# Kernel tuning notes

Measured on AMD Instinct MI355X. Metric: run time of the kernel, lower is better.

## Reference

```python
import jax, jax.numpy as jnp
import numpy as np

N, E = 50000, 800000
IN, H, C = 256, 8, 32  # heads=8, hidden_dim=32 -> out dim 256
NEG_SLOPE = 0.2
EPS = 1e-5


def setup_inputs() -> dict:
    key = jax.random.key(0)
    ks = jax.random.split(key, 6)
    x = jax.random.normal(ks[0], (N, IN), jnp.float32)
    edge_index = jax.random.randint(ks[1], (2, E), 0, N, dtype=jnp.int32)
    W = jax.random.normal(ks[2], (IN, H * C), jnp.float32) / np.sqrt(IN).astype(np.float32)
    att_src = jax.random.normal(ks[3], (H, C), jnp.float32) * 0.1
    att_dst = jax.random.normal(ks[4], (H, C), jnp.float32) * 0.1
    bias = jnp.zeros((H * C,), jnp.float32)
    gamma = jnp.ones((H * C,), jnp.float32)
    beta = jnp.zeros((H * C,), jnp.float32)
    return {"x": x, "edge_index": edge_index, "W": W, "att_src": att_src,
            "att_dst": att_dst, "bias": bias, "gamma": gamma, "beta": beta}


def reference(x, edge_index, W, att_src, att_dst, bias, gamma, beta):
    n = x.shape[0]
    # Linear projection -> per-head features [N, H, C]
    xl = (x @ W).reshape(n, H, C)
    # Per-node attention half-logits [N, H]
    a_src = jnp.einsum('nhc,hc->nh', xl, att_src)
    a_dst = jnp.einsum('nhc,hc->nh', xl, att_dst)
    # Add self loops (PyG GATConv default)
    loops = jnp.arange(n, dtype=edge_index.dtype)
    src = jnp.concatenate([edge_index[0], loops])  # [E+N]
    dst = jnp.concatenate([edge_index[1], loops])
    # Edge attention logits + segment softmax over destination neighborhoods
    logits = jax.nn.leaky_relu(a_src[src] + a_dst[dst], NEG_SLOPE)  # [E+N, H]
    seg_max = jax.ops.segment_max(logits, dst, num_segments=n)
    ex = jnp.exp(logits - seg_max[dst])
    denom = jax.ops.segment_sum(ex, dst, num_segments=n)
    alpha = ex / denom[dst]  # [E+N, H]
    # Weighted scatter-aggregation of source features
    msgs = xl[src] * alpha[:, :, None]  # [E+N, H, C]
    out = jax.ops.segment_sum(msgs, dst, num_segments=n).reshape(n, H * C) + bias
    # LayerNorm over feature dim
    mu = jnp.mean(out, axis=-1, keepdims=True)
    var = jnp.var(out, axis=-1, keepdims=True)
    return (out - mu) / jnp.sqrt(var + EPS) * gamma + beta
```

## Files before the change

kernel.cpp:

```cpp
#include <hip/hip_runtime.h>
#include <math.h>

#define NEG 0.2f
#define LNEPS 1e-5f
#define GB 512

typedef __attribute__((ext_vector_type(8))) short bf16x8;
typedef __attribute__((ext_vector_type(8))) unsigned short u16x8;
typedef __attribute__((ext_vector_type(4))) float f32x4;
typedef __attribute__((ext_vector_type(4))) unsigned int u32x4;

__device__ __forceinline__ float lrelu(float x){ return x > 0.f ? x : NEG*x; }

__device__ __forceinline__ short f2b(float f){
  unsigned u = __float_as_uint(f);
  unsigned r = u + 0x7fffu + ((u >> 16) & 1u);
  return (short)(r >> 16);
}
__device__ __forceinline__ float b2f(unsigned short u){
  return __uint_as_float(((unsigned)u) << 16);
}
__device__ __forceinline__ unsigned cvtpk(float lo, float hi){
  unsigned r;
  asm("v_cvt_pk_bf16_f32 %0, %1, %2" : "=v"(r) : "v"(lo), "v"(hi));
  return r;
}

__global__ __launch_bounds__(256) void wt_k(const float* __restrict__ W,
                                            const float* __restrict__ att_src,
                                            const float* __restrict__ att_dst,
                                            const int* __restrict__ dst,
                                            unsigned short* __restrict__ WTp,
                                            unsigned short* __restrict__ WSp,
                                            int* __restrict__ deg, int E){
  int b = blockIdx.x;
  int tid = threadIdx.x;
  if (b < 32){
    int g = b*256 + tid;
    int l = g & 63;
    int s = (g>>6) & 7;
    int j = (g>>9) & 3;
    int w = g >> 11;
    int col = w*64 + j*16 + (l & 15);
    int kb  = s*32 + (l>>4)*8;
    u16x8 v;
    #pragma unroll
    for (int e=0;e<8;e++) v[e] = (unsigned short)f2b(W[(size_t)(kb+e)*256 + col]);
    *(u16x8*)(WTp + (size_t)g*8) = v;
  } else if (b < 34){
    int g = (b-32)*256 + tid;
    int l = g & 63;
    int s = g >> 6;
    int col = l & 15;
    int kb  = s*32 + (l>>4)*8;
    int head = col & 7;
    const float* av = (col < 8 ? att_src : att_dst) + head*32;
    u16x8 v;
    #pragma unroll
    for (int e=0;e<8;e++){
      const float* wr = W + (size_t)(kb+e)*256 + head*32;
      float sum = 0.f;
      #pragma unroll
      for (int c2=0;c2<32;c2++) sum += wr[c2]*av[c2];
      v[e] = (unsigned short)f2b(sum);
    }
    *(u16x8*)(WSp + (size_t)g*8) = v;
  } else {
    int e = (b-34)*256 + tid;
    if (e < E) atomicAdd(&deg[dst[e]], 1);
  }
}

__global__ __launch_bounds__(1024) void scan1_k(const int* __restrict__ deg,
                                                int* __restrict__ off,
                                                int* __restrict__ bsum, int n){
  __shared__ int wsum[16];
  int tid=threadIdx.x, lane=tid&63, wid=tid>>6;
  int i = blockIdx.x*1024 + tid;
  int v = (i<n)?(deg[i]+1):0;
  int x = v;
  #pragma unroll
  for (int s=1;s<64;s<<=1){ int t2=__shfl_up(x,s); if (lane>=s) x+=t2; }
  if (lane==63) wsum[wid]=x;
  __syncthreads();
  if (tid<16){
    int y=wsum[tid];
    #pragma unroll
    for (int s=1;s<16;s<<=1){ int t2=__shfl_up(y,s); if (tid>=s) y+=t2; }
    wsum[tid]=y;
  }
  __syncthreads();
  int prefix=(wid? wsum[wid-1]:0);
  if (i<n) off[i]=prefix + x - v;
  if (tid==0) bsum[blockIdx.x]=wsum[15];
}

__global__ __launch_bounds__(1024) void scan3self_k(int* __restrict__ off,
    const int* __restrict__ bsum, int* __restrict__ sorted, int* __restrict__ cur,
    int n, int total){
  __shared__ int prefs;
  if (threadIdx.x < 64){
    int v = ((int)threadIdx.x < blockIdx.x) ? bsum[threadIdx.x] : 0;
    #pragma unroll
    for (int s=1;s<64;s<<=1) v += __shfl_xor(v, s);
    if (threadIdx.x==0) prefs = v;
  }
  __syncthreads();
  int i = blockIdx.x*1024 + threadIdx.x;
  if (blockIdx.x==0 && threadIdx.x==0) off[n] = total;
  if (i>=n) return;
  int o = off[i] + prefs;
  off[i] = o;
  sorted[o] = i;
  cur[i] = 1;
}

__device__ __forceinline__ void load_tile(float4 v[4], const float* __restrict__ A,
                                          int t, int M, int tid){
  const float* base = A + (size_t)t*4096;
  int rmax = M - 1 - t*16;
  #pragma unroll
  for (int j=0;j<4;j++){
    int idx4 = (j>>1)*512 + 2*tid + (j&1);
    int r = idx4 >> 6;
    if (r > rmax) idx4 = (rmax<<6) | (idx4 & 63);
    v[j] = *(const float4*)(base + (size_t)idx4*4);
  }
}

__global__ __launch_bounds__(256, 2) void gemm_scat_k(const float* __restrict__ A,
    const unsigned short* __restrict__ WTp, const unsigned short* __restrict__ WSp,
    unsigned short* __restrict__ Cb, float* __restrict__ asd, int M, int nTiles,
    const int* __restrict__ src, const int* __restrict__ dst,
    const int* __restrict__ off, int* __restrict__ cur,
    int* __restrict__ sorted, int E){
  __shared__ __align__(16) unsigned short Asb[16*256];
  int tid = threadIdx.x;

  if (blockIdx.x >= GB){
    int e = (blockIdx.x - GB)*256 + tid;
    if (e < E){
      int d = dst[e];
      int pos = off[d] + atomicAdd(&cur[d], 1);
      sorted[pos] = src[e];
    }
    return;
  }

  int w   = tid >> 6;
  int l   = tid & 63;
  int l15 = l & 15;
  int kg  = l >> 4;
  int colbase = w*64;

  bf16x8 bfr[4][8];
  #pragma unroll
  for (int j=0;j<4;j++)
    #pragma unroll
    for (int ks=0;ks<8;ks++)
      bfr[j][ks] = *(const bf16x8*)(WTp + ((size_t)(((w*4+j)*8+ks)*64 + l))*8);

  bf16x8 bfa[8];
  if (w==0){
    #pragma unroll
    for (int ks=0;ks<8;ks++)
      bfa[ks] = *(const bf16x8*)(WSp + ((size_t)(ks*64 + l))*8);
  }

  int t = blockIdx.x;
  if (t >= nTiles) return;
  float4 v[4];
  load_tile(v, A, t, M, tid);

  while (t < nTiles){
    __syncthreads();
    #pragma unroll
    for (int p=0;p<2;p++){
      u32x4 q;
      q.x = cvtpk(v[2*p].x,   v[2*p].y);
      q.y = cvtpk(v[2*p].z,   v[2*p].w);
      q.z = cvtpk(v[2*p+1].x, v[2*p+1].y);
      q.w = cvtpk(v[2*p+1].z, v[2*p+1].w);
      int slot = p*256 + tid;
      int sw = slot ^ ((slot>>5)&7);
      *(u32x4*)(Asb + (size_t)sw*8) = q;
    }
    __syncthreads();

    int tn = t + GB;
    if (tn < nTiles) load_tile(v, A, tn, M, tid);

    f32x4 acc[4];
    #pragma unroll
    for (int j=0;j<4;j++) acc[j] = (f32x4){0.f,0.f,0.f,0.f};
    f32x4 acc_a = (f32x4){0.f,0.f,0.f,0.f};

    #pragma unroll
    for (int s=0;s<8;s++){
      int slot = l15*32 + kg + s*4;
      int sw = slot ^ (l15 & 7);
      bf16x8 af = *(const bf16x8*)(Asb + (size_t)sw*8);
      #pragma unroll
      for (int j=0;j<4;j++)
        acc[j] = __builtin_amdgcn_mfma_f32_16x16x32_bf16(bfr[j][s], af, acc[j], 0, 0, 0);
      if (w==0)
        acc_a = __builtin_amdgcn_mfma_f32_16x16x32_bf16(bfa[s], af, acc_a, 0, 0, 0);
    }

    int row = t*16 + l15;
    if (row < M){
      unsigned short* cp = Cb + (size_t)row*256 + colbase + kg*4;
      #pragma unroll
      for (int j=0;j<4;j++){
        uint2 pk;
        pk.x = cvtpk(acc[j][0], acc[j][1]);
        pk.y = cvtpk(acc[j][2], acc[j][3]);
        *(uint2*)(cp + j*16) = pk;
      }
      if (w==0){
        float4 av = {acc_a[0], acc_a[1], acc_a[2], acc_a[3]};
        *(float4*)(asd + (size_t)row*16 + kg*4) = av;
      }
    }
    t = tn;
  }
}

__global__ __launch_bounds__(256) void agg5_k(const unsigned short* __restrict__ xlb,
    const float* __restrict__ asd,
    const int* __restrict__ off, const int* __restrict__ sorted,
    const float* __restrict__ bias, const float* __restrict__ gamma,
    const float* __restrict__ beta, float* __restrict__ out, int n){
  int node = blockIdx.x*4 + (threadIdx.x>>6);
  if (node >= n) return;
  int lane = threadIdx.x & 63;
  int half = lane >> 5;
  int sl   = lane & 31;
  int h    = sl >> 2;
  int hh   = lane & 7;
  int je   = lane >> 3;
  float adst_h = asd[(size_t)node*16 + 8 + h];
  float adst_e = asd[(size_t)node*16 + 8 + hh];
  int s0 = off[node], dd = off[node+1] - s0;

  float acc[8] = {0.f,0.f,0.f,0.f,0.f,0.f,0.f,0.f};
  float den = 0.f;

  int i = 0;
  for (; i+8 <= dd; i += 8){
    int s[4];
    #pragma unroll
    for (int j=0;j<4;j++) s[j] = sorted[s0 + i + 2*j + half];
    int se = sorted[s0 + i + je];
    float w_l = __expf(lrelu(asd[(size_t)se*16 + hh] + adst_e));
    float wv[4];
    #pragma unroll
    for (int j=0;j<4;j++) wv[j] = __shfl(w_l, ((2*j+half)<<3) | h);
    u16x8 u[4];
    #pragma unroll
    for (int j=0;j<4;j++) u[j] = *(const u16x8*)(xlb + (size_t)s[j]*256 + sl*8);
    #pragma unroll
    for (int j=0;j<4;j++){
      den += wv[j];
      #pragma unroll
      for (int k=0;k<8;k++) acc[k] += wv[j]*b2f((unsigned short)u[j][k]);
    }
  }
  for (; i < dd; i += 2){
    int idx = i + half;
    bool ok = idx < dd;
    int s1 = ok ? sorted[s0+idx] : node;
    float w1 = ok ? __expf(lrelu(asd[(size_t)s1*16 + h] + adst_h)) : 0.f;
    u16x8 u1 = *(const u16x8*)(xlb + (size_t)s1*256 + sl*8);
    den += w1;
    #pragma unroll
    for (int k=0;k<8;k++) acc[k] += w1*b2f((unsigned short)u1[k]);
  }

  den += __shfl_xor(den, 32);
  #pragma unroll
  for (int k=0;k<8;k++) acc[k] += __shfl_xor(acc[k], 32);

  float rd = 1.0f/den;
  float4 bia0 = *(const float4*)(bias + sl*8);
  float4 bia1 = *(const float4*)(bias + sl*8 + 4);
  float o[8];
  o[0]=acc[0]*rd+bia0.x; o[1]=acc[1]*rd+bia0.y; o[2]=acc[2]*rd+bia0.z; o[3]=acc[3]*rd+bia0.w;
  o[4]=acc[4]*rd+bia1.x; o[5]=acc[5]*rd+bia1.y; o[6]=acc[6]*rd+bia1.z; o[7]=acc[7]*rd+bia1.w;

  float sum=0.f, ssq=0.f;
  #pragma unroll
  for (int k=0;k<8;k++){ sum += o[k]; ssq += o[k]*o[k]; }
  #pragma unroll
  for (int s=1;s<32;s<<=1){ sum += __shfl_xor(sum,s); ssq += __shfl_xor(ssq,s); }
  float mean = sum*(1.0f/256.0f);
  float var  = ssq*(1.0f/256.0f) - mean*mean;
  float rstd = rsqrtf(var + LNEPS);

  int f = sl*8 + half*4;
  float4 g  = *(const float4*)(gamma + f);
  float4 be = *(const float4*)(beta + f);
  int kb = half*4;
  float4 ov;
  ov.x = (o[kb+0]-mean)*rstd*g.x+be.x;
  ov.y = (o[kb+1]-mean)*rstd*g.y+be.y;
  ov.z = (o[kb+2]-mean)*rstd*g.z+be.z;
  ov.w = (o[kb+3]-mean)*rstd*g.w+be.w;
  *(float4*)(out + (size_t)node*256 + f) = ov;
}

extern "C" void kernel_launch(void* const* d_in, const int* in_sizes, int n_in,
                              void* d_out, int out_size, void* d_ws, size_t ws_size,
                              hipStream_t stream){
  const float* x       = (const float*)d_in[0];
  const int*   ei      = (const int*)  d_in[1];
  const float* W       = (const float*)d_in[2];
  const float* att_src = (const float*)d_in[3];
  const float* att_dst = (const float*)d_in[4];
  const float* bias    = (const float*)d_in[5];
  const float* gamma   = (const float*)d_in[6];
  const float* beta    = (const float*)d_in[7];
  float* out = (float*)d_out;

  int N = in_sizes[0]/256;
  int E = in_sizes[1]/2;
  const int* srcp = ei;
  const int* dstp = ei + E;

  unsigned short* xlb = (unsigned short*)d_ws;
  float* asd   = (float*)(xlb + (size_t)N*256);
  int*   deg   = (int*)(asd + (size_t)N*16);
  int*   off   = deg + N;
  int*   cur   = off + N + 1;
  int*   sorted= cur + N;
  int*   bsum  = sorted + E + N;
  unsigned short* WTp = (unsigned short*)(bsum + 1024);
  unsigned short* WSp = WTp + 65536;

  int nb = (N + 1023)/1024;
  int nTiles = (N + 15)/16;
  int scatBlocks = (E + 255)/256;

  hipMemsetAsync(deg, 0, (size_t)N*sizeof(int), stream);
  wt_k<<<34 + scatBlocks, 256, 0, stream>>>(W, att_src, att_dst, dstp, WTp, WSp, deg, E);
  scan1_k<<<nb, 1024, 0, stream>>>(deg, off, bsum, N);
  scan3self_k<<<nb, 1024, 0, stream>>>(off, bsum, sorted, cur, N, E + N);
  gemm_scat_k<<<GB + scatBlocks, 256, 0, stream>>>(x, WTp, WSp, xlb, asd, N, nTiles,
                                                   srcp, dstp, off, cur, sorted, E);
  agg5_k<<<(N+3)/4, 256, 0, stream>>>(xlb, asd, off, sorted, bias, gamma, beta, out, N);
}
```

Before: 187.1 us.

## Load GEMM A fragments directly into registers and split attention logits arrays

The GEMM now has each lane read its own row fragment of x straight from global memory into MFMA operand registers. This removes the LDS staging buffer and both block barriers, and the K dimension is processed in two halves so the next half's load overlaps the current MFMAs. The per-node attention logits are stored as separate a_src and a_dst arrays of 8 floats each instead of one interleaved 16-float record, so the gather in aggregation touches a denser array. The price is more register pressure from holding 8 float4 per lane, and less coalesced global reads of x.

```diff
diff --git a/kernel.cpp b/kernel.cpp
--- a/kernel.cpp
+++ b/kernel.cpp
@@ -115,26 +115,32 @@
   cur[i] = 1;
 }
 
-__device__ __forceinline__ void load_tile(float4 v[4], const float* __restrict__ A,
-                                          int t, int M, int tid){
-  const float* base = A + (size_t)t*4096;
-  int rmax = M - 1 - t*16;
-  #pragma unroll
-  for (int j=0;j<4;j++){
-    int idx4 = (j>>1)*512 + 2*tid + (j&1);
-    int r = idx4 >> 6;
-    if (r > rmax) idx4 = (rmax<<6) | (idx4 & 63);
-    v[j] = *(const float4*)(base + (size_t)idx4*4);
+__device__ __forceinline__ void load_half(float4 nx[8], const float* p){
+  #pragma unroll
+  for (int s=0;s<4;s++){
+    nx[2*s]   = *(const float4*)(p + s*32);
+    nx[2*s+1] = *(const float4*)(p + s*32 + 4);
+  }
+}
+__device__ __forceinline__ void cvt_half(bf16x8 af[4], const float4 nx[8]){
+  #pragma unroll
+  for (int s=0;s<4;s++){
+    u32x4 q;
+    q.x = cvtpk(nx[2*s].x,   nx[2*s].y);
+    q.y = cvtpk(nx[2*s].z,   nx[2*s].w);
+    q.z = cvtpk(nx[2*s+1].x, nx[2*s+1].y);
+    q.w = cvtpk(nx[2*s+1].z, nx[2*s+1].w);
+    af[s] = __builtin_bit_cast(bf16x8, q);
   }
 }
 
 __global__ __launch_bounds__(256, 2) void gemm_scat_k(const float* __restrict__ A,
     const unsigned short* __restrict__ WTp, const unsigned short* __restrict__ WSp,
-    unsigned short* __restrict__ Cb, float* __restrict__ asd, int M, int nTiles,
+    unsigned short* __restrict__ Cb,
+    float* __restrict__ a_src, float* __restrict__ a_dst, int M, int nTiles,
     const int* __restrict__ src, const int* __restrict__ dst,
     const int* __restrict__ off, int* __restrict__ cur,
     int* __restrict__ sorted, int E){
-  __shared__ __align__(16) unsigned short Asb[16*256];
   int tid = threadIdx.x;
 
   if (blockIdx.x >= GB){
@@ -169,42 +175,42 @@
 
   int t = blockIdx.x;
   if (t >= nTiles) return;
-  float4 v[4];
-  load_tile(v, A, t, M, tid);
+  int row0 = t*16 + l15;
+  const float* ap = A + (size_t)(row0 < M ? row0 : M-1)*256 + kg*8;
+  float4 nx[8];
+  load_half(nx, ap);
 
   while (t < nTiles){
-    __syncthreads();
-    #pragma unroll
-    for (int p=0;p<2;p++){
-      u32x4 q;
-      q.x = cvtpk(v[2*p].x,   v[2*p].y);
-      q.y = cvtpk(v[2*p].z,   v[2*p].w);
-      q.z = cvtpk(v[2*p+1].x, v[2*p+1].y);
-      q.w = cvtpk(v[2*p+1].z, v[2*p+1].w);
-      int slot = p*256 + tid;
-      int sw = slot ^ ((slot>>5)&7);
-      *(u32x4*)(Asb + (size_t)sw*8) = q;
-    }
-    __syncthreads();
-
-    int tn = t + GB;
-    if (tn < nTiles) load_tile(v, A, tn, M, tid);
-
     f32x4 acc[4];
     #pragma unroll
     for (int j=0;j<4;j++) acc[j] = (f32x4){0.f,0.f,0.f,0.f};
     f32x4 acc_a = (f32x4){0.f,0.f,0.f,0.f};
-
-    #pragma unroll
-    for (int s=0;s<8;s++){
-      int slot = l15*32 + kg + s*4;
-      int sw = slot ^ (l15 & 7);
-      bf16x8 af = *(const bf16x8*)(Asb + (size_t)sw*8);
+    bf16x8 af[4];
+
+    cvt_half(af, nx);
+    load_half(nx, ap + 128);
+    #pragma unroll
+    for (int s=0;s<4;s++){
       #pragma unroll
       for (int j=0;j<4;j++)
-        acc[j] = __builtin_amdgcn_mfma_f32_16x16x32_bf16(bfr[j][s], af, acc[j], 0, 0, 0);
+        acc[j] = __builtin_amdgcn_mfma_f32_16x16x32_bf16(bfr[j][s], af[s], acc[j], 0, 0, 0);
       if (w==0)
-        acc_a = __builtin_amdgcn_mfma_f32_16x16x32_bf16(bfa[s], af, acc_a, 0, 0, 0);
+        acc_a = __builtin_amdgcn_mfma_f32_16x16x32_bf16(bfa[s], af[s], acc_a, 0, 0, 0);
+    }
+
+    int tn = t + GB;
+    int rown = tn < nTiles ? tn*16 + l15 : row0;
+    const float* apn = A + (size_t)(rown < M ? rown : M-1)*256 + kg*8;
+
+    cvt_half(af, nx);
+    load_half(nx, apn);
+    #pragma unroll
+    for (int s=0;s<4;s++){
+      #pragma unroll
+      for (int j=0;j<4;j++)
+        acc[j] = __builtin_amdgcn_mfma_f32_16x16x32_bf16(bfr[j][4+s], af[s], acc[j], 0, 0, 0);
+      if (w==0)
+        acc_a = __builtin_amdgcn_mfma_f32_16x16x32_bf16(bfa[4+s], af[s], acc_a, 0, 0, 0);
     }
 
     int row = t*16 + l15;
@@ -219,15 +225,16 @@
       }
       if (w==0){
         float4 av = {acc_a[0], acc_a[1], acc_a[2], acc_a[3]};
-        *(float4*)(asd + (size_t)row*16 + kg*4) = av;
+        float* dstp2 = (kg < 2 ? a_src : a_dst) + (size_t)row*8 + (kg&1)*4;
+        *(float4*)dstp2 = av;
       }
     }
-    t = tn;
+    t = tn; row0 = rown; ap = apn;
   }
 }
 
 __global__ __launch_bounds__(256) void agg5_k(const unsigned short* __restrict__ xlb,
-    const float* __restrict__ asd,
+    const float* __restrict__ a_src, const float* __restrict__ a_dst,
     const int* __restrict__ off, const int* __restrict__ sorted,
     const float* __restrict__ bias, const float* __restrict__ gamma,
     const float* __restrict__ beta, float* __restrict__ out, int n){
@@ -239,8 +246,8 @@
   int h    = sl >> 2;
   int hh   = lane & 7;
   int je   = lane >> 3;
-  float adst_h = asd[(size_t)node*16 + 8 + h];
-  float adst_e = asd[(size_t)node*16 + 8 + hh];
+  float adst_h = a_dst[(size_t)node*8 + h];
+  float adst_e = a_dst[(size_t)node*8 + hh];
   int s0 = off[node], dd = off[node+1] - s0;
 
   float acc[8] = {0.f,0.f,0.f,0.f,0.f,0.f,0.f,0.f};
@@ -252,7 +259,7 @@
     #pragma unroll
     for (int j=0;j<4;j++) s[j] = sorted[s0 + i + 2*j + half];
     int se = sorted[s0 + i + je];
-    float w_l = __expf(lrelu(asd[(size_t)se*16 + hh] + adst_e));
+    float w_l = __expf(lrelu(a_src[(size_t)se*8 + hh] + adst_e));
     float wv[4];
     #pragma unroll
     for (int j=0;j<4;j++) wv[j] = __shfl(w_l, ((2*j+half)<<3) | h);
@@ -270,7 +277,7 @@
     int idx = i + half;
     bool ok = idx < dd;
     int s1 = ok ? sorted[s0+idx] : node;
-    float w1 = ok ? __expf(lrelu(asd[(size_t)s1*16 + h] + adst_h)) : 0.f;
+    float w1 = ok ? __expf(lrelu(a_src[(size_t)s1*8 + h] + adst_h)) : 0.f;
     u16x8 u1 = *(const u16x8*)(xlb + (size_t)s1*256 + sl*8);
     den += w1;
     #pragma unroll
@@ -328,8 +335,9 @@
   const int* dstp = ei + E;
 
   unsigned short* xlb = (unsigned short*)d_ws;
-  float* asd   = (float*)(xlb + (size_t)N*256);
-  int*   deg   = (int*)(asd + (size_t)N*16);
+  float* a_src = (float*)(xlb + (size_t)N*256);
+  float* a_dst = a_src + (size_t)N*8;
+  int*   deg   = (int*)(a_dst + (size_t)N*8);
   int*   off   = deg + N;
   int*   cur   = off + N + 1;
   int*   sorted= cur + N;
@@ -345,7 +353,8 @@
   wt_k<<<34 + scatBlocks, 256, 0, stream>>>(W, att_src, att_dst, dstp, WTp, WSp, deg, E);
   scan1_k<<<nb, 1024, 0, stream>>>(deg, off, bsum, N);
   scan3self_k<<<nb, 1024, 0, stream>>>(off, bsum, sorted, cur, N, E + N);
-  gemm_scat_k<<<GB + scatBlocks, 256, 0, stream>>>(x, WTp, WSp, xlb, asd, N, nTiles,
-                                                   srcp, dstp, off, cur, sorted, E);
-  agg5_k<<<(N+3)/4, 256, 0, stream>>>(xlb, asd, off, sorted, bias, gamma, beta, out, N);
-}
+  gemm_scat_k<<<GB + scatBlocks, 256, 0, stream>>>(x, WTp, WSp, xlb, a_src, a_dst,
+                                                   N, nTiles, srcp, dstp, off, cur,
+                                                   sorted, E);
+  agg5_k<<<(N+3)/4, 256, 0, stream>>>(xlb, a_src, a_dst, off, sorted, bias, gamma, beta, out, N);
+}
```

Result: no change. 188.5 us (+0.7%).

## Split attention logits into separate src/dst arrays and double GEMM grid

Applied to the files above, without the earlier changes.

The per-node attention half-logits move from one interleaved [N,16] array into two separate [N,8] arrays, a_src and a_dst. The gather of source logits in aggregation then touches a denser 32-byte row per neighbor instead of a 64-byte stride, which shrinks the cache footprint of the random gathers. Separately, the GEMM persistent grid grows from 512 to 1024 blocks, so each block handles fewer tiles. The larger grid may reduce per-block latency hiding through prefetch but adds more resident blocks competing with the scatter blocks.

```diff
diff --git a/kernel.cpp b/kernel.cpp
--- a/kernel.cpp
+++ b/kernel.cpp
@@ -3,7 +3,7 @@
 
 #define NEG 0.2f
 #define LNEPS 1e-5f
-#define GB 512
+#define GBN 1024
 
 typedef __attribute__((ext_vector_type(8))) short bf16x8;
 typedef __attribute__((ext_vector_type(8))) unsigned short u16x8;
@@ -130,15 +130,16 @@
 
 __global__ __launch_bounds__(256, 2) void gemm_scat_k(const float* __restrict__ A,
     const unsigned short* __restrict__ WTp, const unsigned short* __restrict__ WSp,
-    unsigned short* __restrict__ Cb, float* __restrict__ asd, int M, int nTiles,
+    unsigned short* __restrict__ Cb,
+    float* __restrict__ a_src, float* __restrict__ a_dst, int M, int nTiles,
     const int* __restrict__ src, const int* __restrict__ dst,
     const int* __restrict__ off, int* __restrict__ cur,
     int* __restrict__ sorted, int E){
   __shared__ __align__(16) unsigned short Asb[16*256];
   int tid = threadIdx.x;
 
-  if (blockIdx.x >= GB){
-    int e = (blockIdx.x - GB)*256 + tid;
+  if (blockIdx.x >= GBN){
+    int e = (blockIdx.x - GBN)*256 + tid;
     if (e < E){
       int d = dst[e];
       int pos = off[d] + atomicAdd(&cur[d], 1);
@@ -187,7 +188,7 @@
     }
     __syncthreads();
 
-    int tn = t + GB;
+    int tn = t + GBN;
     if (tn < nTiles) load_tile(v, A, tn, M, tid);
 
     f32x4 acc[4];
@@ -219,7 +220,8 @@
       }
       if (w==0){
         float4 av = {acc_a[0], acc_a[1], acc_a[2], acc_a[3]};
-        *(float4*)(asd + (size_t)row*16 + kg*4) = av;
+        float* dstp2 = (kg < 2 ? a_src : a_dst) + (size_t)row*8 + (kg&1)*4;
+        *(float4*)dstp2 = av;
       }
     }
     t = tn;
@@ -227,7 +229,7 @@
 }
 
 __global__ __launch_bounds__(256) void agg5_k(const unsigned short* __restrict__ xlb,
-    const float* __restrict__ asd,
+    const float* __restrict__ a_src, const float* __restrict__ a_dst,
     const int* __restrict__ off, const int* __restrict__ sorted,
     const float* __restrict__ bias, const float* __restrict__ gamma,
     const float* __restrict__ beta, float* __restrict__ out, int n){
@@ -239,8 +241,8 @@
   int h    = sl >> 2;
   int hh   = lane & 7;
   int je   = lane >> 3;
-  float adst_h = asd[(size_t)node*16 + 8 + h];
-  float adst_e = asd[(size_t)node*16 + 8 + hh];
+  float adst_h = a_dst[(size_t)node*8 + h];
+  float adst_e = a_dst[(size_t)node*8 + hh];
   int s0 = off[node], dd = off[node+1] - s0;
 
   float acc[8] = {0.f,0.f,0.f,0.f,0.f,0.f,0.f,0.f};
@@ -252,7 +254,7 @@
     #pragma unroll
     for (int j=0;j<4;j++) s[j] = sorted[s0 + i + 2*j + half];
     int se = sorted[s0 + i + je];
-    float w_l = __expf(lrelu(asd[(size_t)se*16 + hh] + adst_e));
+    float w_l = __expf(lrelu(a_src[(size_t)se*8 + hh] + adst_e));
     float wv[4];
     #pragma unroll
     for (int j=0;j<4;j++) wv[j] = __shfl(w_l, ((2*j+half)<<3) | h);
@@ -270,7 +272,7 @@
     int idx = i + half;
     bool ok = idx < dd;
     int s1 = ok ? sorted[s0+idx] : node;
-    float w1 = ok ? __expf(lrelu(asd[(size_t)s1*16 + h] + adst_h)) : 0.f;
+    float w1 = ok ? __expf(lrelu(a_src[(size_t)s1*8 + h] + adst_h)) : 0.f;
     u16x8 u1 = *(const u16x8*)(xlb + (size_t)s1*256 + sl*8);
     den += w1;
     #pragma unroll
@@ -328,8 +330,9 @@
   const int* dstp = ei + E;
 
   unsigned short* xlb = (unsigned short*)d_ws;
-  float* asd   = (float*)(xlb + (size_t)N*256);
-  int*   deg   = (int*)(asd + (size_t)N*16);
+  float* a_src = (float*)(xlb + (size_t)N*256);
+  float* a_dst = a_src + (size_t)N*8;
+  int*   deg   = (int*)(a_dst + (size_t)N*8);
   int*   off   = deg + N;
   int*   cur   = off + N + 1;
   int*   sorted= cur + N;
@@ -345,7 +348,8 @@
   wt_k<<<34 + scatBlocks, 256, 0, stream>>>(W, att_src, att_dst, dstp, WTp, WSp, deg, E);
   scan1_k<<<nb, 1024, 0, stream>>>(deg, off, bsum, N);
   scan3self_k<<<nb, 1024, 0, stream>>>(off, bsum, sorted, cur, N, E + N);
-  gemm_scat_k<<<GB + scatBlocks, 256, 0, stream>>>(x, WTp, WSp, xlb, asd, N, nTiles,
-                                                   srcp, dstp, off, cur, sorted, E);
-  agg5_k<<<(N+3)/4, 256, 0, stream>>>(xlb, asd, off, sorted, bias, gamma, beta, out, N);
-}
+  gemm_scat_k<<<GBN + scatBlocks, 256, 0, stream>>>(x, WTp, WSp, xlb, a_src, a_dst,
+                                                    N, nTiles, srcp, dstp, off, cur,
+                                                    sorted, E);
+  agg5_k<<<(N+3)/4, 256, 0, stream>>>(xlb, a_src, a_dst, off, sorted, bias, gamma, beta, out, N);
+}
```

Result: no change. 188.1 us (+0.5%).
